# Kernel optimization log

Measured on AMD Instinct MI355X. Metric: run time of the kernel, lower is better.

The kernel has to match this reference:

```python
import jax, jax.numpy as jnp
import numpy as np

N, E, F, S = 20000, 160000, 16, 8
ECC1, ECC2, ECC3 = 40, 24, 24
DS = [96, 256, 768, 512, 64, 1]


def setup_inputs() -> dict:
    key = jax.random.key(0)
    ks = iter(jax.random.split(key, 40))
    inp = {}
    inp["x"] = jax.random.normal(next(ks), (N, F), dtype=jnp.float32)
    inp["edge_index"] = jax.random.randint(next(ks), (E, 2), 0, N, dtype=jnp.int32)
    inp["e"] = jax.random.uniform(next(ks), (E, S), dtype=jnp.float32)

    def dense_p(k, fi, fo):
        return (jax.random.normal(k, (fi, fo), dtype=jnp.float32) * (1.0 / np.sqrt(fi)),
                jnp.zeros((fo,), dtype=jnp.float32))

    # ECCConv params: kernel_network dense (S -> F_in*F_out), root kernel, bias
    for i, (fi, fo) in enumerate([(F, ECC1), (ECC1, ECC2), (ECC2, ECC3)], start=1):
        We, be = dense_p(next(ks), S, fi * fo)
        root, _ = dense_p(next(ks), fi, fo)
        inp[f"We{i}"], inp[f"be{i}"] = We, be
        inp[f"root{i}"], inp[f"b{i}"] = root, jnp.zeros((fo,), dtype=jnp.float32)

    dims = [ECC3] + DS
    for i in range(6):
        W, b = dense_p(next(ks), dims[i], dims[i + 1])
        inp[f"Wd{i+1}"], inp[f"bd{i+1}"] = W, b
    return inp


def _ecc(h, src, tgt, e, We, be, root, b):
    fi, fo = root.shape
    # per-edge filter matrices from edge features: [E, F_in, F_out]
    K = (e @ We + be).reshape(e.shape[0], fi, fo)
    msg = jnp.einsum('ef,efo->eo', h[src], K)          # gather + per-edge matvec
    agg = jax.ops.segment_sum(msg, tgt, num_segments=h.shape[0])  # scatter-add
    return jax.nn.relu(agg + h @ root + b)


def reference(x, edge_index, e,
              We1, be1, root1, b1,
              We2, be2, root2, b2,
              We3, be3, root3, b3,
              Wd1, bd1, Wd2, bd2, Wd3, bd3, Wd4, bd4, Wd5, bd5, Wd6, bd6):
    src, tgt = edge_index[:, 0], edge_index[:, 1]
    h = _ecc(x, src, tgt, e, We1, be1, root1, b1)
    h = _ecc(h, src, tgt, e, We2, be2, root2, b2)
    h = _ecc(h, src, tgt, e, We3, be3, root3, b3)
    g = jnp.sum(h, axis=0, keepdims=True)  # GlobalSumPool (single mode) -> [1, 24]
    for W, b in [(Wd1, bd1), (Wd2, bd2), (Wd3, bd3), (Wd4, bd4), (Wd5, bd5)]:
        g = jax.nn.relu(g @ W + b)
    return g @ Wd6 + bd6  # [1, 1]
```

## Files before the change

kernel.cpp:

```cpp
#include <hip/hip_runtime.h>

constexpr int NN  = 20000;
constexpr int NE  = 160000;
constexpr int CAP = 32;
constexpr int TN2 = 8;
constexpr int NBM = 16;

__device__ inline void gstore(float* p, float v) {
    __hip_atomic_store(p, v, __ATOMIC_RELAXED, __HIP_MEMORY_SCOPE_AGENT);
}
__device__ inline float gload(const float* p) {
    return __hip_atomic_load(p, __ATOMIC_RELAXED, __HIP_MEMORY_SCOPE_AGENT);
}

__device__ inline void mbarrier(int* ctr, int target, bool wait) {
    __syncthreads();
    if (threadIdx.x == 0) {
        __threadfence();
        __hip_atomic_fetch_add(ctr, 1, __ATOMIC_ACQ_REL, __HIP_MEMORY_SCOPE_AGENT);
        if (wait)
            while (__hip_atomic_load(ctr, __ATOMIC_ACQUIRE, __HIP_MEMORY_SCOPE_AGENT) < target) {}
    }
    __syncthreads();
}

template<int FI, int FO2, int CH>
__device__ void stage_half(float* Wh, const float* __restrict__ We,
                           const float* __restrict__ be, const float* __restrict__ root,
                           int c0)
{
    constexpr int O4 = FO2 / 4;
    for (int t = threadIdx.x; t < FI * CH; t += 256) {
        const int f = t / CH, ccp = t % CH, cc = c0 + ccp;
        const int s = cc / O4, oq = cc % O4;
        const float4* src;
        if (s < 8)       src = (const float4*)(We + (size_t)s * FI * FO2 + f * FO2 + oq * 4);
        else if (s == 8) src = (const float4*)(be + f * FO2 + oq * 4);
        else             src = (const float4*)(root + f * FO2 + oq * 4);
        ((float4*)Wh)[t] = *src;
    }
}

template<int FI, int FO2>
__device__ void gemm_half_PL(const float* htile, const float* Wh,
                             const float* __restrict__ bias,
                             float* P_lds, float* __restrict__ seg9g,
                             int n0, int c0)
{
    constexpr int PW = 10 * FO2, C4 = PW / 4, CH = C4 / 2, O4 = FO2 / 4;
    constexpr int PL = 9 * FO2;
    constexpr int TPN = 256 / TN2;
    constexpr int HS  = FI + 4;
    const int nl = threadIdx.x / TPN, lane = threadIdx.x % TPN;
    const float*  hr = &htile[nl * HS];
    const float4* W4 = (const float4*)Wh;
    for (int ccp = lane; ccp < CH; ccp += TPN) {
        const int cc = c0 + ccp;
        float4 a = {0.f, 0.f, 0.f, 0.f};
        #pragma unroll
        for (int f = 0; f < FI; f++) {
            const float  hf = hr[f];
            const float4 w  = W4[f * CH + ccp];
            a.x = fmaf(hf, w.x, a.x); a.y = fmaf(hf, w.y, a.y);
            a.z = fmaf(hf, w.z, a.z); a.w = fmaf(hf, w.w, a.w);
        }
        if (cc < 9 * O4) {
            *(float4*)&P_lds[nl * PL + cc * 4] = a;
        } else {
            const float4 b4 = ((const float4*)bias)[cc - 9 * O4];
            a.x += b4.x; a.y += b4.y; a.z += b4.z; a.w += b4.w;
            *(float4*)&seg9g[(size_t)(n0 + nl) * FO2 + (cc - 9 * O4) * 4] = a;
        }
    }
}

template<int FO2>
__device__ void push_phase(const float* P_lds, const int* __restrict__ cnt_s,
                           const int* __restrict__ se_eid, const float* __restrict__ e,
                           float* __restrict__ msg, float* scratch, int n0)
{
    constexpr int PL = 9 * FO2, OQ2 = FO2 / 4;
    float* elds = scratch;
    int*   esl  = (int*)(scratch + 2048);
    int*   enl  = esl + 256;
    int*   offs = enl + 256;
    const int tid = threadIdx.x;
    if (tid == 0) {
        int a = 0;
        for (int i = 0; i < TN2; i++) { offs[i] = a; a += min(cnt_s[n0 + i], CAP); }
        offs[TN2] = a;
    }
    __syncthreads();
    const int ET = offs[TN2];
    for (int T = tid; T < ET; T += 256) {
        int nl = 0;
        #pragma unroll
        for (int i = 1; i < TN2; i++) nl += (T >= offs[i]);
        const int j    = T - offs[nl];
        const int slot = (n0 + nl) * CAP + j;
        const int eid  = se_eid[slot];
        esl[T] = slot; enl[T] = nl;
        *(float4*)&elds[T * 8]     = *(const float4*)(e + (size_t)eid * 8);
        *(float4*)&elds[T * 8 + 4] = *(const float4*)(e + (size_t)eid * 8 + 4);
    }
    __syncthreads();
    for (int T = tid; T < ET * OQ2; T += 256) {
        const int ed = T / OQ2, oq = T % OQ2;
        const int nl = enl[ed], slot = esl[ed];
        const float* Pr = &P_lds[nl * PL + oq * 4];
        const float* ee = &elds[ed * 8];
        float4 m = *(const float4*)(Pr + 8 * FO2);
        #pragma unroll
        for (int s = 0; s < 8; s++) {
            const float  es = ee[s];
            const float4 w  = *(const float4*)(Pr + s * FO2);
            m.x = fmaf(es, w.x, m.x); m.y = fmaf(es, w.y, m.y);
            m.z = fmaf(es, w.z, m.z); m.w = fmaf(es, w.w, m.w);
        }
        *(float4*)&msg[(size_t)slot * FO2 + oq * 4] = m;
    }
}

__global__ __launch_bounds__(256)
void bucket_kernel(const int* __restrict__ eidx,
                   int* __restrict__ cnt_s, int* __restrict__ cnt_t,
                   int* __restrict__ se_eid, int* __restrict__ te_slot)
{
    const int eid = blockIdx.x * 256 + threadIdx.x;
    const int2 st = ((const int2*)eidx)[eid];
    const int qs = atomicAdd(&cnt_s[st.x], 1);
    if (qs < CAP) {
        se_eid[st.x * CAP + qs] = eid;
        const int qt = atomicAdd(&cnt_t[st.y], 1);
        if (qt < CAP) te_slot[st.y * CAP + qt] = st.x * CAP + qs;
    }
}

__global__ __launch_bounds__(256, 4)
void l1_push_kernel(const float* __restrict__ x,
                    const float* __restrict__ We1, const float* __restrict__ be1,
                    const float* __restrict__ root1, const float* __restrict__ b1,
                    const int* __restrict__ cnt_s, const int* __restrict__ se_eid,
                    const float* __restrict__ e,
                    float* __restrict__ seg9_1, float* __restrict__ msg1)
{
    constexpr int FI = 16, FO2 = 40, CH = 50;
    constexpr int WHF = FI * CH * 4;
    constexpr int PLF = TN2 * 9 * FO2;
    constexpr int HTF = TN2 * (FI + 4);
    __shared__ float smem[WHF + PLF + HTF];
    float* Wh    = smem;
    float* P_lds = smem + WHF;
    float* htile = smem + WHF + PLF;
    const int tid = threadIdx.x;
    const int n0  = blockIdx.x * TN2;

    stage_half<FI, FO2, CH>(Wh, We1, be1, root1, 0);
    for (int t = tid; t < TN2 * 4; t += 256) {
        const int nl = t / 4, fq = t % 4;
        *(float4*)&htile[nl * 20 + fq * 4] =
            *(const float4*)(x + (size_t)(n0 + nl) * 16 + fq * 4);
    }
    __syncthreads();
    gemm_half_PL<FI, FO2>(htile, Wh, b1, P_lds, seg9_1, n0, 0);
    __syncthreads();
    stage_half<FI, FO2, CH>(Wh, We1, be1, root1, CH);
    __syncthreads();
    gemm_half_PL<FI, FO2>(htile, Wh, b1, P_lds, seg9_1, n0, CH);
    __syncthreads();
    push_phase<FO2>(P_lds, cnt_s, se_eid, e, msg1, Wh, n0);
}

template<int FI, int FO2, int J>
__global__ __launch_bounds__(256, 4)
void gather_gemm_push_kernel(const float* __restrict__ msg_prev,
                             const int* __restrict__ cnt_t, const int* __restrict__ te_slot,
                             const float* __restrict__ seg9_prev,
                             const float* __restrict__ We, const float* __restrict__ be,
                             const float* __restrict__ root, const float* __restrict__ bias,
                             const int* __restrict__ cnt_s, const int* __restrict__ se_eid,
                             const float* __restrict__ e,
                             float* __restrict__ seg9_next, float* __restrict__ msg_next)
{
    constexpr int CH  = (10 * FO2 / 4) / 2;
    constexpr int OQi = FI / 4;
    constexpr int HS  = FI + 4;
    constexpr int WHF = FI * CH * 4;
    constexpr int PLF = TN2 * 9 * FO2;
    constexpr int HTF = TN2 * HS;
    __shared__ float smem[WHF + PLF + HTF];
    float* Wh    = smem;
    float* P_lds = smem + WHF;
    float* htile = smem + WHF + PLF;
    const int tid = threadIdx.x;
    const int n0  = blockIdx.x * TN2;

    stage_half<FI, FO2, CH>(Wh, We, be, root, 0);
    for (int t = tid; t < TN2 * OQi; t += 256) {
        const int nl = t / OQi, oq = t % OQi;
        *(float4*)&htile[nl * HS + oq * 4] =
            *(const float4*)(seg9_prev + (size_t)(n0 + nl) * FI + oq * 4);
    }
    __syncthreads();

    for (int T = tid; T < TN2 * OQi * J; T += 256) {
        const int nl = T / (OQi * J), r = T % (OQi * J), oq = r / J, jh = r % J;
        const int n = n0 + nl;
        const int d = min(cnt_t[n], CAP);
        if (jh >= d) continue;
        float4 acc = {0.f, 0.f, 0.f, 0.f};
        const int* tb = te_slot + n * CAP;
        for (int k = jh; k < d; k += J) {
            const int slot = tb[k];
            const float4 v = *(const float4*)(msg_prev + (size_t)slot * FI + oq * 4);
            acc.x += v.x; acc.y += v.y; acc.z += v.z; acc.w += v.w;
        }
        float* hp = &htile[nl * HS + oq * 4];
        atomicAdd(hp + 0, acc.x);
        atomicAdd(hp + 1, acc.y);
        atomicAdd(hp + 2, acc.z);
        atomicAdd(hp + 3, acc.w);
    }
    __syncthreads();
    for (int t = tid; t < TN2 * OQi; t += 256) {
        float4* p = (float4*)&htile[(t / OQi) * HS + (t % OQi) * 4];
        float4 v = *p;
        v.x = fmaxf(v.x, 0.f); v.y = fmaxf(v.y, 0.f);
        v.z = fmaxf(v.z, 0.f); v.w = fmaxf(v.w, 0.f);
        *p = v;
    }
    __syncthreads();

    gemm_half_PL<FI, FO2>(htile, Wh, bias, P_lds, seg9_next, n0, 0);
    __syncthreads();
    stage_half<FI, FO2, CH>(Wh, We, be, root, CH);
    __syncthreads();
    gemm_half_PL<FI, FO2>(htile, Wh, bias, P_lds, seg9_next, n0, CH);
    __syncthreads();
    push_phase<FO2>(P_lds, cnt_s, se_eid, e, msg_next, Wh, n0);
}

__global__ __launch_bounds__(256)
void msg_colsum_kernel(const float* __restrict__ msg, const int* __restrict__ cnt_t,
                       const int* __restrict__ te_slot, const float* __restrict__ seg9,
                       float* __restrict__ g)
{
    constexpr int FO = 24, OQ = 6;
    __shared__ float gl[FO];
    const int tid = threadIdx.x;
    if (tid < FO) gl[tid] = 0.f;
    __syncthreads();
    for (int i = blockIdx.x * 256 + tid; i < NN * OQ; i += gridDim.x * 256) {
        const int n = i / OQ, oq = i - n * OQ;
        float4 acc = *(const float4*)(seg9 + (size_t)n * FO + oq * 4);
        const int d = min(cnt_t[n], CAP);
        const int* tb = te_slot + n * CAP;
        #pragma unroll 2
        for (int k = 0; k < d; k++) {
            const int slot = tb[k];
            const float4 v = *(const float4*)(msg + (size_t)slot * FO + oq * 4);
            acc.x += v.x; acc.y += v.y; acc.z += v.z; acc.w += v.w;
        }
        atomicAdd(&gl[oq * 4 + 0], fmaxf(acc.x, 0.f));
        atomicAdd(&gl[oq * 4 + 1], fmaxf(acc.y, 0.f));
        atomicAdd(&gl[oq * 4 + 2], fmaxf(acc.z, 0.f));
        atomicAdd(&gl[oq * 4 + 3], fmaxf(acc.w, 0.f));
    }
    __syncthreads();
    if (tid < FO) unsafeAtomicAdd(&g[tid], gl[tid]);
}

__global__ __launch_bounds__(256)
void mlp_kernel(const float* __restrict__ g, int* __restrict__ ctr,
                const float* __restrict__ Wd1, const float* __restrict__ bd1,
                const float* __restrict__ Wd2, const float* __restrict__ bd2,
                const float* __restrict__ Wd3, const float* __restrict__ bd3,
                const float* __restrict__ Wd4, const float* __restrict__ bd4,
                const float* __restrict__ Wd5, const float* __restrict__ bd5,
                const float* __restrict__ Wd6, const float* __restrict__ bd6,
                float* __restrict__ m3, float* __restrict__ m4,
                float* __restrict__ out)
{
    __shared__ float v0[768];
    __shared__ float v1[96];
    __shared__ float red[256];
    const int tid = threadIdx.x, b = blockIdx.x;

    if (tid < 24) v0[tid] = g[tid];
    __syncthreads();
    if (tid < 96) {
        float a = bd1[tid];
        #pragma unroll
        for (int i = 0; i < 24; i++) a = fmaf(v0[i], Wd1[i * 96 + tid], a);
        v1[tid] = fmaxf(a, 0.f);
    }
    __syncthreads();
    {
        float a = bd2[tid];
        #pragma unroll
        for (int i = 0; i < 96; i++) a = fmaf(v1[i], Wd2[i * 256 + tid], a);
        red[tid] = fmaxf(a, 0.f);
    }
    __syncthreads();
    v0[tid] = red[tid];
    __syncthreads();

    if (tid < 192) {
        const int o = b * 48 + (tid % 48), kg = tid / 48;
        float a = 0.f;
        #pragma unroll 8
        for (int i = kg * 64; i < kg * 64 + 64; i++)
            a = fmaf(v0[i], Wd3[(size_t)i * 768 + o], a);
        red[tid] = a;
    }
    __syncthreads();
    if (tid < 48) {
        float s = bd3[b * 48 + tid] + red[tid] + red[48 + tid] + red[96 + tid] + red[144 + tid];
        gstore(&m3[b * 48 + tid], fmaxf(s, 0.f));
    }
    mbarrier(ctr, 1 * NBM, true);

    for (int i = tid; i < 768; i += 256) v0[i] = gload(&m3[i]);
    __syncthreads();
    {
        const int o = b * 32 + (tid & 31), kg = tid >> 5;
        float a = 0.f;
        #pragma unroll 8
        for (int i = kg * 96; i < kg * 96 + 96; i++)
            a = fmaf(v0[i], Wd4[(size_t)i * 512 + o], a);
        red[tid] = a;
    }
    __syncthreads();
    if (tid < 32) {
        float s = bd4[b * 32 + tid];
        #pragma unroll
        for (int k = 0; k < 8; k++) s += red[k * 32 + tid];
        gstore(&m4[b * 32 + tid], fmaxf(s, 0.f));
    }
    mbarrier(ctr, 2 * NBM, b == 0);

    if (b == 0) {
        for (int i = tid; i < 512; i += 256) v0[i] = gload(&m4[i]);
        __syncthreads();
        {
            const int o = tid & 63, kg = tid >> 6;
            float a = 0.f;
            #pragma unroll 8
            for (int i = kg * 128; i < kg * 128 + 128; i++)
                a = fmaf(v0[i], Wd5[(size_t)i * 64 + o], a);
            red[tid] = a;
        }
        __syncthreads();
        if (tid < 64) {
            float s = bd5[tid] + red[tid] + red[64 + tid] + red[128 + tid] + red[192 + tid];
            float v = fmaxf(s, 0.f) * Wd6[tid];
            #pragma unroll
            for (int off = 32; off > 0; off >>= 1)
                v += __shfl_down(v, off, 64);
            if (tid == 0) out[0] = v + bd6[0];
        }
    }
}

extern "C" void kernel_launch(void* const* d_in, const int* in_sizes, int n_in,
                              void* d_out, int out_size, void* d_ws, size_t ws_size,
                              hipStream_t stream)
{
    const float* x     = (const float*)d_in[0];
    const int*   eidx  = (const int*)  d_in[1];
    const float* e     = (const float*)d_in[2];
    const float* We1   = (const float*)d_in[3];  const float* be1 = (const float*)d_in[4];
    const float* root1 = (const float*)d_in[5];  const float* b1  = (const float*)d_in[6];
    const float* We2   = (const float*)d_in[7];  const float* be2 = (const float*)d_in[8];
    const float* root2 = (const float*)d_in[9];  const float* b2  = (const float*)d_in[10];
    const float* We3   = (const float*)d_in[11]; const float* be3 = (const float*)d_in[12];
    const float* root3 = (const float*)d_in[13]; const float* b3  = (const float*)d_in[14];
    const float* Wd1 = (const float*)d_in[15]; const float* bd1 = (const float*)d_in[16];
    const float* Wd2 = (const float*)d_in[17]; const float* bd2 = (const float*)d_in[18];
    const float* Wd3 = (const float*)d_in[19]; const float* bd3 = (const float*)d_in[20];
    const float* Wd4 = (const float*)d_in[21]; const float* bd4 = (const float*)d_in[22];
    const float* Wd5 = (const float*)d_in[23]; const float* bd5 = (const float*)d_in[24];
    const float* Wd6 = (const float*)d_in[25]; const float* bd6 = (const float*)d_in[26];

    int*   wi      = (int*)d_ws;
    float* wf      = (float*)d_ws;
    int*   cnt_s   = wi;
    int*   cnt_t   = wi + 20000;
    float* g       = wf + 40000;
    int*   mctr    = wi + 40064;
    float* m3      = wf + 40096;
    float* m4      = m3 + 768;
    int*   se_eid  = wi + 41376;
    int*   te_slot = wi + 681376;
    float* seg9_1  = wf + 1321376;
    float* seg9_2  = wf + 2121376;
    float* seg9_3  = wf + 2601376;
    float* msg1    = wf + 3081376;
    float* msg3    = msg1;
    float* msg2    = wf + 28681376;

    hipMemsetAsync(d_ws, 0, (size_t)41376 * sizeof(float), stream);

    bucket_kernel<<<625, 256, 0, stream>>>(eidx, cnt_s, cnt_t, se_eid, te_slot);

    l1_push_kernel<<<NN / TN2, 256, 0, stream>>>(x, We1, be1, root1, b1,
                                                 cnt_s, se_eid, e, seg9_1, msg1);

    gather_gemm_push_kernel<40, 24, 3><<<NN / TN2, 256, 0, stream>>>(
        msg1, cnt_t, te_slot, seg9_1, We2, be2, root2, b2,
        cnt_s, se_eid, e, seg9_2, msg2);

    gather_gemm_push_kernel<24, 24, 5><<<NN / TN2, 256, 0, stream>>>(
        msg2, cnt_t, te_slot, seg9_2, We3, be3, root3, b3,
        cnt_s, se_eid, e, seg9_3, msg3);

    msg_colsum_kernel<<<512, 256, 0, stream>>>(msg3, cnt_t, te_slot, seg9_3, g);

    mlp_kernel<<<NBM, 256, 0, stream>>>(g, mctr,
                                        Wd1, bd1, Wd2, bd2, Wd3, bd3,
                                        Wd4, bd4, Wd5, bd5, Wd6, bd6,
                                        m3, m4, (float*)d_out);
}
```

Measured before the change: 258.3 us.

## Pre-sort edge features by source slot and flatten per-edge gather across block

New measurement: 310.4 us. +20.2%, slower.

```diff
diff --git a/kernel.cpp b/kernel.cpp
--- a/kernel.cpp
+++ b/kernel.cpp
@@ -41,14 +41,12 @@
     }
 }
 
-template<int FI, int FO2>
-__device__ void gemm_half_PL(const float* htile, const float* Wh,
-                             const float* __restrict__ bias,
-                             float* P_lds, float* __restrict__ seg9g,
-                             int n0, int c0)
-{
-    constexpr int PW = 10 * FO2, C4 = PW / 4, CH = C4 / 2, O4 = FO2 / 4;
-    constexpr int PL = 9 * FO2;
+template<int FI, int FO2, int CH>
+__device__ void gemm_PL(const float* htile, const float* Wh,
+                        const float* __restrict__ bias,
+                        float* P_lds, float* __restrict__ seg9g, int n0, int c0)
+{
+    constexpr int O4 = FO2 / 4, PL = 9 * FO2;
     constexpr int TPN = 256 / TN2;
     constexpr int HS  = FI + 4;
     const int nl = threadIdx.x / TPN, lane = threadIdx.x % TPN;
@@ -75,33 +73,25 @@
 }
 
 template<int FO2>
-__device__ void push_phase(const float* P_lds, const int* __restrict__ cnt_s,
-                           const int* __restrict__ se_eid, const float* __restrict__ e,
-                           float* __restrict__ msg, float* scratch, int n0)
+__device__ void push_phase(const float* P_lds, const int* offs_s,
+                           const float* __restrict__ esort, float* __restrict__ msg,
+                           float* scratch, int n0)
 {
     constexpr int PL = 9 * FO2, OQ2 = FO2 / 4;
     float* elds = scratch;
     int*   esl  = (int*)(scratch + 2048);
     int*   enl  = esl + 256;
-    int*   offs = enl + 256;
     const int tid = threadIdx.x;
-    if (tid == 0) {
-        int a = 0;
-        for (int i = 0; i < TN2; i++) { offs[i] = a; a += min(cnt_s[n0 + i], CAP); }
-        offs[TN2] = a;
-    }
-    __syncthreads();
-    const int ET = offs[TN2];
+    const int ET = offs_s[TN2];
     for (int T = tid; T < ET; T += 256) {
         int nl = 0;
         #pragma unroll
-        for (int i = 1; i < TN2; i++) nl += (T >= offs[i]);
-        const int j    = T - offs[nl];
+        for (int i = 1; i < TN2; i++) nl += (T >= offs_s[i]);
+        const int j    = T - offs_s[nl];
         const int slot = (n0 + nl) * CAP + j;
-        const int eid  = se_eid[slot];
         esl[T] = slot; enl[T] = nl;
-        *(float4*)&elds[T * 8]     = *(const float4*)(e + (size_t)eid * 8);
-        *(float4*)&elds[T * 8 + 4] = *(const float4*)(e + (size_t)eid * 8 + 4);
+        *(float4*)&elds[T * 8]     = *(const float4*)(esort + (size_t)slot * 8);
+        *(float4*)&elds[T * 8 + 4] = *(const float4*)(esort + (size_t)slot * 8 + 4);
     }
     __syncthreads();
     for (int T = tid; T < ET * OQ2; T += 256) {
@@ -122,26 +112,28 @@
 }
 
 __global__ __launch_bounds__(256)
-void bucket_kernel(const int* __restrict__ eidx,
+void bucket_kernel(const int* __restrict__ eidx, const float* __restrict__ e,
                    int* __restrict__ cnt_s, int* __restrict__ cnt_t,
-                   int* __restrict__ se_eid, int* __restrict__ te_slot)
+                   int* __restrict__ te_slot, float* __restrict__ esort)
 {
     const int eid = blockIdx.x * 256 + threadIdx.x;
     const int2 st = ((const int2*)eidx)[eid];
     const int qs = atomicAdd(&cnt_s[st.x], 1);
     if (qs < CAP) {
-        se_eid[st.x * CAP + qs] = eid;
+        const int slot = st.x * CAP + qs;
+        const float4* e4 = (const float4*)(e + (size_t)eid * 8);
+        *(float4*)&esort[(size_t)slot * 8]     = e4[0];
+        *(float4*)&esort[(size_t)slot * 8 + 4] = e4[1];
         const int qt = atomicAdd(&cnt_t[st.y], 1);
-        if (qt < CAP) te_slot[st.y * CAP + qt] = st.x * CAP + qs;
-    }
-}
-
-__global__ __launch_bounds__(256, 4)
+        if (qt < CAP) te_slot[st.y * CAP + qt] = slot;
+    }
+}
+
+__global__ __launch_bounds__(256, 6)
 void l1_push_kernel(const float* __restrict__ x,
                     const float* __restrict__ We1, const float* __restrict__ be1,
                     const float* __restrict__ root1, const float* __restrict__ b1,
-                    const int* __restrict__ cnt_s, const int* __restrict__ se_eid,
-                    const float* __restrict__ e,
+                    const int* __restrict__ cnt_s, const float* __restrict__ esort,
                     float* __restrict__ seg9_1, float* __restrict__ msg1)
 {
     constexpr int FI = 16, FO2 = 40, CH = 50;
@@ -149,12 +141,18 @@
     constexpr int PLF = TN2 * 9 * FO2;
     constexpr int HTF = TN2 * (FI + 4);
     __shared__ float smem[WHF + PLF + HTF];
+    __shared__ int offs_s[TN2 + 1];
     float* Wh    = smem;
     float* P_lds = smem + WHF;
     float* htile = smem + WHF + PLF;
     const int tid = threadIdx.x;
     const int n0  = blockIdx.x * TN2;
 
+    if (tid == 0) {
+        int a = 0;
+        for (int i = 0; i < TN2; i++) { offs_s[i] = a; a += min(cnt_s[n0 + i], CAP); }
+        offs_s[TN2] = a;
+    }
     stage_half<FI, FO2, CH>(Wh, We1, be1, root1, 0);
     for (int t = tid; t < TN2 * 4; t += 256) {
         const int nl = t / 4, fq = t % 4;
@@ -162,40 +160,52 @@
             *(const float4*)(x + (size_t)(n0 + nl) * 16 + fq * 4);
     }
     __syncthreads();
-    gemm_half_PL<FI, FO2>(htile, Wh, b1, P_lds, seg9_1, n0, 0);
+    gemm_PL<FI, FO2, CH>(htile, Wh, b1, P_lds, seg9_1, n0, 0);
     __syncthreads();
     stage_half<FI, FO2, CH>(Wh, We1, be1, root1, CH);
     __syncthreads();
-    gemm_half_PL<FI, FO2>(htile, Wh, b1, P_lds, seg9_1, n0, CH);
-    __syncthreads();
-    push_phase<FO2>(P_lds, cnt_s, se_eid, e, msg1, Wh, n0);
-}
-
-template<int FI, int FO2, int J>
-__global__ __launch_bounds__(256, 4)
+    gemm_PL<FI, FO2, CH>(htile, Wh, b1, P_lds, seg9_1, n0, CH);
+    __syncthreads();
+    push_phase<FO2>(P_lds, offs_s, esort, msg1, Wh, n0);
+}
+
+template<int FI, int FO2, int CHP>
+__global__ __launch_bounds__(256, 6)
 void gather_gemm_push_kernel(const float* __restrict__ msg_prev,
                              const int* __restrict__ cnt_t, const int* __restrict__ te_slot,
                              const float* __restrict__ seg9_prev,
                              const float* __restrict__ We, const float* __restrict__ be,
                              const float* __restrict__ root, const float* __restrict__ bias,
-                             const int* __restrict__ cnt_s, const int* __restrict__ se_eid,
-                             const float* __restrict__ e,
+                             const int* __restrict__ cnt_s, const float* __restrict__ esort,
                              float* __restrict__ seg9_next, float* __restrict__ msg_next)
 {
-    constexpr int CH  = (10 * FO2 / 4) / 2;
-    constexpr int OQi = FI / 4;
-    constexpr int HS  = FI + 4;
-    constexpr int WHF = FI * CH * 4;
-    constexpr int PLF = TN2 * 9 * FO2;
-    constexpr int HTF = TN2 * HS;
+    constexpr int C4    = 10 * FO2 / 4;
+    constexpr int NPASS = C4 / CHP;
+    constexpr int OQi   = FI / 4, HS = FI + 4;
+    constexpr int WHF   = FI * CHP * 4;
+    constexpr int PLF   = TN2 * 9 * FO2;
+    constexpr int HTF   = TN2 * HS;
     __shared__ float smem[WHF + PLF + HTF];
+    __shared__ int tslot[TN2 * CAP];
+    __shared__ int offs_t[TN2 + 1], offs_s[TN2 + 1];
     float* Wh    = smem;
     float* P_lds = smem + WHF;
     float* htile = smem + WHF + PLF;
     const int tid = threadIdx.x;
     const int n0  = blockIdx.x * TN2;
 
-    stage_half<FI, FO2, CH>(Wh, We, be, root, 0);
+    if (tid == 0) {
+        int a = 0;
+        for (int i = 0; i < TN2; i++) { offs_t[i] = a; a += min(cnt_t[n0 + i], CAP); }
+        offs_t[TN2] = a;
+    }
+    if (tid == 64) {
+        int a = 0;
+        for (int i = 0; i < TN2; i++) { offs_s[i] = a; a += min(cnt_s[n0 + i], CAP); }
+        offs_s[TN2] = a;
+    }
+    for (int t = tid; t < TN2 * CAP; t += 256) tslot[t] = te_slot[n0 * CAP + t];
+    stage_half<FI, FO2, CHP>(Wh, We, be, root, 0);
     for (int t = tid; t < TN2 * OQi; t += 256) {
         const int nl = t / OQi, oq = t % OQi;
         *(float4*)&htile[nl * HS + oq * 4] =
@@ -203,23 +213,20 @@
     }
     __syncthreads();
 
-    for (int T = tid; T < TN2 * OQi * J; T += 256) {
-        const int nl = T / (OQi * J), r = T % (OQi * J), oq = r / J, jh = r % J;
-        const int n = n0 + nl;
-        const int d = min(cnt_t[n], CAP);
-        if (jh >= d) continue;
-        float4 acc = {0.f, 0.f, 0.f, 0.f};
-        const int* tb = te_slot + n * CAP;
-        for (int k = jh; k < d; k += J) {
-            const int slot = tb[k];
-            const float4 v = *(const float4*)(msg_prev + (size_t)slot * FI + oq * 4);
-            acc.x += v.x; acc.y += v.y; acc.z += v.z; acc.w += v.w;
-        }
+    const int ETt = offs_t[TN2];
+    for (int T = tid; T < ETt * OQi; T += 256) {
+        const int ed = T / OQi, oq = T % OQi;
+        int nl = 0;
+        #pragma unroll
+        for (int i = 1; i < TN2; i++) nl += (ed >= offs_t[i]);
+        const int k    = ed - offs_t[nl];
+        const int slot = tslot[nl * CAP + k];
+        const float4 v = *(const float4*)(msg_prev + (size_t)slot * FI + oq * 4);
         float* hp = &htile[nl * HS + oq * 4];
-        atomicAdd(hp + 0, acc.x);
-        atomicAdd(hp + 1, acc.y);
-        atomicAdd(hp + 2, acc.z);
-        atomicAdd(hp + 3, acc.w);
+        atomicAdd(hp + 0, v.x);
+        atomicAdd(hp + 1, v.y);
+        atomicAdd(hp + 2, v.z);
+        atomicAdd(hp + 3, v.w);
     }
     __syncthreads();
     for (int t = tid; t < TN2 * OQi; t += 256) {
@@ -231,13 +238,17 @@
     }
     __syncthreads();
 
-    gemm_half_PL<FI, FO2>(htile, Wh, bias, P_lds, seg9_next, n0, 0);
-    __syncthreads();
-    stage_half<FI, FO2, CH>(Wh, We, be, root, CH);
-    __syncthreads();
-    gemm_half_PL<FI, FO2>(htile, Wh, bias, P_lds, seg9_next, n0, CH);
-    __syncthreads();
-    push_phase<FO2>(P_lds, cnt_s, se_eid, e, msg_next, Wh, n0);
+    #pragma unroll
+    for (int p = 0; p < NPASS; p++) {
+        if (p > 0) {
+            __syncthreads();
+            stage_half<FI, FO2, CHP>(Wh, We, be, root, p * CHP);
+            __syncthreads();
+        }
+        gemm_PL<FI, FO2, CHP>(htile, Wh, bias, P_lds, seg9_next, n0, p * CHP);
+    }
+    __syncthreads();
+    push_phase<FO2>(P_lds, offs_s, esort, msg_next, Wh, n0);
 }
 
 __global__ __launch_bounds__(256)
@@ -245,26 +256,47 @@
                        const int* __restrict__ te_slot, const float* __restrict__ seg9,
                        float* __restrict__ g)
 {
-    constexpr int FO = 24, OQ = 6;
+    constexpr int FO = 24, OQ = 6, HS = 28;
+    __shared__ float htile[TN2 * HS];
+    __shared__ int tslot[TN2 * CAP];
+    __shared__ int offs_t[TN2 + 1];
     __shared__ float gl[FO];
     const int tid = threadIdx.x;
-    if (tid < FO) gl[tid] = 0.f;
-    __syncthreads();
-    for (int i = blockIdx.x * 256 + tid; i < NN * OQ; i += gridDim.x * 256) {
-        const int n = i / OQ, oq = i - n * OQ;
-        float4 acc = *(const float4*)(seg9 + (size_t)n * FO + oq * 4);
-        const int d = min(cnt_t[n], CAP);
-        const int* tb = te_slot + n * CAP;
-        #pragma unroll 2
-        for (int k = 0; k < d; k++) {
-            const int slot = tb[k];
-            const float4 v = *(const float4*)(msg + (size_t)slot * FO + oq * 4);
-            acc.x += v.x; acc.y += v.y; acc.z += v.z; acc.w += v.w;
-        }
-        atomicAdd(&gl[oq * 4 + 0], fmaxf(acc.x, 0.f));
-        atomicAdd(&gl[oq * 4 + 1], fmaxf(acc.y, 0.f));
-        atomicAdd(&gl[oq * 4 + 2], fmaxf(acc.z, 0.f));
-        atomicAdd(&gl[oq * 4 + 3], fmaxf(acc.w, 0.f));
+    const int n0  = blockIdx.x * TN2;
+
+    if (tid == 0) {
+        int a = 0;
+        for (int i = 0; i < TN2; i++) { offs_t[i] = a; a += min(cnt_t[n0 + i], CAP); }
+        offs_t[TN2] = a;
+    }
+    if (tid >= 64 && tid < 64 + FO) gl[tid - 64] = 0.f;
+    for (int t = tid; t < TN2 * CAP; t += 256) tslot[t] = te_slot[n0 * CAP + t];
+    for (int t = tid; t < TN2 * OQ; t += 256) {
+        const int nl = t / OQ, oq = t % OQ;
+        *(float4*)&htile[nl * HS + oq * 4] =
+            *(const float4*)(seg9 + (size_t)(n0 + nl) * FO + oq * 4);
+    }
+    __syncthreads();
+
+    const int ETt = offs_t[TN2];
+    for (int T = tid; T < ETt * OQ; T += 256) {
+        const int ed = T / OQ, oq = T % OQ;
+        int nl = 0;
+        #pragma unroll
+        for (int i = 1; i < TN2; i++) nl += (ed >= offs_t[i]);
+        const int k    = ed - offs_t[nl];
+        const int slot = tslot[nl * CAP + k];
+        const float4 v = *(const float4*)(msg + (size_t)slot * FO + oq * 4);
+        float* hp = &htile[nl * HS + oq * 4];
+        atomicAdd(hp + 0, v.x);
+        atomicAdd(hp + 1, v.y);
+        atomicAdd(hp + 2, v.z);
+        atomicAdd(hp + 3, v.w);
+    }
+    __syncthreads();
+    for (int t = tid; t < TN2 * FO; t += 256) {
+        const int nl = t / FO, o = t % FO;
+        atomicAdd(&gl[o], fmaxf(htile[nl * HS + o], 0.f));
     }
     __syncthreads();
     if (tid < FO) unsafeAtomicAdd(&g[tid], gl[tid]);
@@ -390,31 +422,31 @@
     int*   mctr    = wi + 40064;
     float* m3      = wf + 40096;
     float* m4      = m3 + 768;
-    int*   se_eid  = wi + 41376;
-    int*   te_slot = wi + 681376;
-    float* seg9_1  = wf + 1321376;
-    float* seg9_2  = wf + 2121376;
-    float* seg9_3  = wf + 2601376;
-    float* msg1    = wf + 3081376;
+    int*   te_slot = wi + 41376;
+    float* esort   = wf + 681376;
+    float* seg9_1  = wf + 5801376;
+    float* seg9_2  = wf + 6601376;
+    float* seg9_3  = wf + 7081376;
+    float* msg1    = wf + 7561376;
     float* msg3    = msg1;
-    float* msg2    = wf + 28681376;
+    float* msg2    = wf + 33161376;
 
     hipMemsetAsync(d_ws, 0, (size_t)41376 * sizeof(float), stream);
 
-    bucket_kernel<<<625, 256, 0, stream>>>(eidx, cnt_s, cnt_t, se_eid, te_slot);
+    bucket_kernel<<<625, 256, 0, stream>>>(eidx, e, cnt_s, cnt_t, te_slot, esort);
 
     l1_push_kernel<<<NN / TN2, 256, 0, stream>>>(x, We1, be1, root1, b1,
-                                                 cnt_s, se_eid, e, seg9_1, msg1);
-
-    gather_gemm_push_kernel<40, 24, 3><<<NN / TN2, 256, 0, stream>>>(
+                                                 cnt_s, esort, seg9_1, msg1);
+
+    gather_gemm_push_kernel<40, 24, 30><<<NN / TN2, 256, 0, stream>>>(
         msg1, cnt_t, te_slot, seg9_1, We2, be2, root2, b2,
-        cnt_s, se_eid, e, seg9_2, msg2);
-
-    gather_gemm_push_kernel<24, 24, 5><<<NN / TN2, 256, 0, stream>>>(
+        cnt_s, esort, seg9_2, msg2);
+
+    gather_gemm_push_kernel<24, 24, 60><<<NN / TN2, 256, 0, stream>>>(
         msg2, cnt_t, te_slot, seg9_2, We3, be3, root3, b3,
-        cnt_s, se_eid, e, seg9_3, msg3);
-
-    msg_colsum_kernel<<<512, 256, 0, stream>>>(msg3, cnt_t, te_slot, seg9_3, g);
+        cnt_s, esort, seg9_3, msg3);
+
+    msg_colsum_kernel<<<NN / TN2, 256, 0, stream>>>(msg3, cnt_t, te_slot, seg9_3, g);
 
     mlp_kernel<<<NBM, 256, 0, stream>>>(g, mctr,
                                         Wd1, bd1, Wd2, bd2, Wd3, bd3,
```
